# Kernel tuning notes

Measured on AMD Instinct MI355X. Metric: run time of the kernel, lower is better.

Reference implementation:

```python
import jax, jax.numpy as jnp
import numpy as np

IN_FEATURES = 4096
OUT_FEATURES = 4096


def fht(x):
    """Normalized fast Walsh-Hadamard transform along last axis (n = power of 2).
    Equals x @ H_n / sqrt(n); matches matmul_hadU(t)_cuda when had_K is None (K=1)."""
    n = x.shape[-1]
    orig_shape = x.shape
    x = x.reshape(-1, n)
    h = 1
    while h < n:
        x = x.reshape(-1, n // (2 * h), 2, h)
        a = x[:, :, 0, :]
        b = x[:, :, 1, :]
        x = jnp.stack([a + b, a - b], axis=2).reshape(-1, n)
        h *= 2
    scale = jnp.asarray(1.0 / np.sqrt(n), dtype=x.dtype)
    return (x * scale).reshape(orig_shape)


def decode_e8p(Qidxs, grid_abs):
    """E8P12-style decode: each 16-bit codeword -> 8 fp16 weights.
    Low 8 bits index a 256-entry table of 8 absolute values; high 8 bits are
    per-element sign flips. Returns dense W of shape [out, in]."""
    idx = Qidxs.astype(jnp.int32) & 0xFFFF            # [out, in/8]
    abs_vals = grid_abs[idx & 0xFF]                   # [out, in/8, 8]
    sbits = (idx[..., None] >> (8 + jnp.arange(8, dtype=jnp.int32))) & 1
    signs = (1 - 2 * sbits).astype(grid_abs.dtype)    # [out, in/8, 8] in {+1,-1}
    w = abs_vals * signs
    return w.reshape(Qidxs.shape[0], -1)              # [out, in]


def setup_inputs() -> dict:
    key = jax.random.key(0)
    k1, k2, k3, k4, k5, k6 = jax.random.split(key, 6)
    inp = {}
    inp["input"] = jax.random.normal(k1, (2, 4096, IN_FEATURES), dtype=jnp.float16)
    inp["Qidxs"] = jax.random.randint(k2, (OUT_FEATURES, IN_FEATURES // 8), 0, 65536, dtype=jnp.int32)
    # abs half-integer-ish grid values (E8 lattice magnitudes live in ~[0.25, 3.75])
    inp["grid_abs"] = (jax.random.uniform(k3, (256, 8), dtype=jnp.float32) * 3.0 + 0.25).astype(jnp.float16)
    # SU/SV are random sign vectors in QuIP
    inp["SU"] = (1 - 2 * jax.random.bernoulli(k4, 0.5, (IN_FEATURES,)).astype(jnp.float16))
    inp["SV"] = (1 - 2 * jax.random.bernoulli(k5, 0.5, (OUT_FEATURES,)).astype(jnp.float16))
    inp["Wscale"] = jnp.ones((), dtype=jnp.float32)
    inp["bias"] = jax.random.normal(k6, (OUT_FEATURES,), dtype=jnp.float16) * jnp.float16(0.01)
    return inp


def reference(input, Qidxs, grid_abs, SU, SV, Wscale, bias):
    x = input.reshape(-1, input.shape[-1])            # [T, in]
    x = x * SU                                        # input sign rescale
    x = fht(x)                                        # H^T x / sqrt(n) (H symmetric)
    x = (x * Wscale).astype(jnp.float16)              # global weight scale
    W = decode_e8p(Qidxs, grid_abs)                   # [out, in] dequantized lattice weights
    out = jnp.dot(x, W.T, preferred_element_type=jnp.float32).astype(jnp.float16)  # [T, out]
    out = fht(out)                                    # output Hadamard
    out = out * SV + bias                             # output sign rescale + bias
    return out.reshape(*input.shape[:-1], out.shape[-1])
```

## Files before the change

kernel.cpp:

```cpp
#include <hip/hip_runtime.h>
#include <hip/hip_bf16.h>
#include <stdint.h>

typedef _Float16 f16;
typedef _Float16 f16x8 __attribute__((ext_vector_type(8)));
typedef float f32x4 __attribute__((ext_vector_type(4)));

#define N_FEAT 4096
#define M_ROWS 8192
#define QSTRIDE 512

#define GLD16(gptr, lptr)                                                      \
  __builtin_amdgcn_global_load_lds(                                            \
      (const __attribute__((address_space(1))) void*)(gptr),                   \
      (__attribute__((address_space(3))) void*)(uint32_t)(uintptr_t)(lptr),    \
      16, 0, 0)

#define PAD64(i) ((i) + (((i) >> 6) << 2))

__device__ __forceinline__ void fht16(float v[16]) {
#pragma unroll
  for (int h = 1; h < 16; h <<= 1) {
#pragma unroll
    for (int i = 0; i < 16; i += (h << 1)) {
#pragma unroll
      for (int j = 0; j < h; ++j) {
        float a = v[i + j], b = v[i + j + h];
        v[i + j] = a + b;
        v[i + j + h] = a - b;
      }
    }
  }
}

__device__ __forceinline__ void fht16v(f32x4 v[16]) {
#pragma unroll
  for (int h = 1; h < 16; h <<= 1) {
#pragma unroll
    for (int i = 0; i < 16; i += (h << 1)) {
#pragma unroll
      for (int j = 0; j < h; ++j) {
        f32x4 a = v[i + j], b = v[i + j + h];
        v[i + j] = a + b;
        v[i + j + h] = a - b;
      }
    }
  }
}

__device__ __forceinline__ void fht4(float& a, float& b, float& c, float& d) {
  float t0 = a + b, t1 = a - b, t2 = c + d, t3 = c - d;
  a = t0 + t2; b = t1 + t3; c = t0 - t2; d = t1 - t3;
}

#define SWZ(c) ((c) ^ (((((c) >> 4) ^ ((c) >> 8)) & 7) << 2))

__global__ __launch_bounds__(256) void k_fht_in(const float* __restrict__ x,
                                                const float* __restrict__ SU,
                                                const float* __restrict__ wscale,
                                                f16* __restrict__ out) {
  __shared__ __attribute__((aligned(16))) float lds[4 * 4096];
  const int t = threadIdx.x;
  const int rw = t >> 6;
  const int u = t & 63;
  const size_t row = (size_t)blockIdx.x * 4 + rw;
  float* pl = &lds[rw << 12];
  const float* xr = x + row * N_FEAT;

#pragma unroll
  for (int g = 0; g < 4; ++g) {
    const int c16 = (g << 10) + (u << 4);
    float v[16];
#pragma unroll
    for (int q = 0; q < 4; ++q) {
      const f32x4 a = *(const f32x4*)(xr + c16 + (q << 2));
      const f32x4 s4 = *(const f32x4*)(SU + c16 + (q << 2));
      const f32x4 m = a * s4;
      v[4 * q + 0] = m[0]; v[4 * q + 1] = m[1];
      v[4 * q + 2] = m[2]; v[4 * q + 3] = m[3];
    }
    fht16(v);
#pragma unroll
    for (int q = 0; q < 4; ++q) {
      const int col = c16 + (q << 2);
      f32x4 wv = {v[4 * q + 0], v[4 * q + 1], v[4 * q + 2], v[4 * q + 3]};
      *(f32x4*)&pl[SWZ(col)] = wv;
    }
  }
  __syncthreads();

  {
    const int b = u >> 2, a4 = (u & 3) << 2;
    f32x4 v[16];
#pragma unroll
    for (int jj = 0; jj < 16; ++jj)
      v[jj] = *(const f32x4*)&pl[SWZ((b << 8) + (jj << 4) + a4)];
    fht16v(v);
#pragma unroll
    for (int jj = 0; jj < 16; ++jj)
      *(f32x4*)&pl[SWZ((b << 8) + (jj << 4) + a4)] = v[jj];
  }
  __syncthreads();

  {
    const int q4 = u << 2;
    f32x4 v[16];
#pragma unroll
    for (int j = 0; j < 16; ++j)
      v[j] = *(const f32x4*)&pl[SWZ((j << 8) + q4)];
    fht16v(v);
    const float s = wscale[0] * 0.015625f;
    f16* op = out + row * N_FEAT;
#pragma unroll
    for (int j = 0; j < 16; ++j) {
      union { f16 h[4]; uint2 u2; } pk;
      pk.h[0] = (f16)(v[j][0] * s); pk.h[1] = (f16)(v[j][1] * s);
      pk.h[2] = (f16)(v[j][2] * s); pk.h[3] = (f16)(v[j][3] * s);
      *(uint2*)(op + (j << 8) + q4) = pk.u2;
    }
  }
}

__global__ __launch_bounds__(256) void k_wA(const int* __restrict__ q,
                                            const float* __restrict__ grid,
                                            f16* __restrict__ Wp) {
  __shared__ float tabf[2048];
  __shared__ float tile[64 * 65];
  const int t = threadIdx.x;
  const int kg = blockIdx.x;
  const int ng = blockIdx.y;
  {
    *(float4*)&tabf[t * 8] = *(const float4*)(grid + t * 8);
    *(float4*)&tabf[t * 8 + 4] = *(const float4*)(grid + t * 8 + 4);
  }
  __syncthreads();

#pragma unroll
  for (int e2 = 0; e2 < 2; ++e2) {
    const int e = t + (e2 << 8);
    const int nl = e >> 3, c = e & 7;
    const unsigned code =
        (unsigned)q[(size_t)(ng * 64 + nl) * QSTRIDE + kg * 8 + c] & 0xffffu;
    const float* tb = &tabf[(code & 255u) * 8];
#pragma unroll
    for (int j = 0; j < 8; ++j) {
      const int bi = __float_as_int(tb[j]) ^ (int)(((code >> (8 + j)) & 1u) << 31);
      tile[nl * 65 + (c << 3) + j] = __int_as_float(bi);
    }
  }
  __syncthreads();

  {
    const int k = t & 63, p = t >> 6;
    float v[16];
#pragma unroll
    for (int j = 0; j < 16; ++j) v[j] = tile[(16 * p + j) * 65 + k];
    fht16(v);
#pragma unroll
    for (int j = 0; j < 16; ++j) tile[(16 * p + j) * 65 + k] = v[j];
  }
  __syncthreads();

  {
    const int k = t & 63, base = (t >> 6) << 2;
#pragma unroll
    for (int bb = 0; bb < 4; ++bb) {
      const int low = base + bb;
      float v0 = tile[(low) * 65 + k],      v1 = tile[(low + 16) * 65 + k];
      float v2 = tile[(low + 32) * 65 + k], v3 = tile[(low + 48) * 65 + k];
      fht4(v0, v1, v2, v3);
      tile[(low) * 65 + k] = v0;      tile[(low + 16) * 65 + k] = v1;
      tile[(low + 32) * 65 + k] = v2; tile[(low + 48) * 65 + k] = v3;
    }
  }
  __syncthreads();

  {
    const int nl = t >> 2, koff = (t & 3) << 4;
    union { f16 h[16]; int4 v[2]; } u;
#pragma unroll
    for (int i = 0; i < 16; ++i) u.h[i] = (f16)tile[nl * 65 + koff + i];
    int4* dst = (int4*)(Wp + (size_t)(ng * 64 + nl) * N_FEAT + kg * 64 + koff);
    dst[0] = u.v[0];
    dst[1] = u.v[1];
  }
}

__global__ __launch_bounds__(256) void k_wB(f16* __restrict__ Wp) {
  __shared__ float tile[64 * 65];
  const int t = threadIdx.x;
  const int kg = blockIdx.x;
  const int n0 = blockIdx.y;
  {
    const int n1 = t >> 2, koff = (t & 3) << 4;
    const f16* src = Wp + (size_t)(n0 + 64 * n1) * N_FEAT + kg * 64 + koff;
    union { f16 h[16]; int4 v[2]; } u;
    u.v[0] = ((const int4*)src)[0];
    u.v[1] = ((const int4*)src)[1];
#pragma unroll
    for (int i = 0; i < 16; ++i) tile[n1 * 65 + koff + i] = (float)u.h[i];
  }
  __syncthreads();
  {
    const int k = t & 63, p = t >> 6;
    float v[16];
#pragma unroll
    for (int j = 0; j < 16; ++j) v[j] = tile[(16 * p + j) * 65 + k];
    fht16(v);
#pragma unroll
    for (int j = 0; j < 16; ++j) tile[(16 * p + j) * 65 + k] = v[j];
  }
  __syncthreads();
  {
    const int k = t & 63, base = (t >> 6) << 2;
#pragma unroll
    for (int bb = 0; bb < 4; ++bb) {
      const int low = base + bb;
      float v0 = tile[(low) * 65 + k],      v1 = tile[(low + 16) * 65 + k];
      float v2 = tile[(low + 32) * 65 + k], v3 = tile[(low + 48) * 65 + k];
      fht4(v0, v1, v2, v3);
      tile[(low) * 65 + k] = v0;      tile[(low + 16) * 65 + k] = v1;
      tile[(low + 32) * 65 + k] = v2; tile[(low + 48) * 65 + k] = v3;
    }
  }
  __syncthreads();
  {
    const int n1 = t >> 2, koff = (t & 3) << 4;
    union { f16 h[16]; int4 v[2]; } u;
#pragma unroll
    for (int i = 0; i < 16; ++i) u.h[i] = (f16)tile[n1 * 65 + koff + i];
    int4* dst = (int4*)(Wp + (size_t)(n0 + 64 * n1) * N_FEAT + kg * 64 + koff);
    dst[0] = u.v[0];
    dst[1] = u.v[1];
  }
}

#define BM 256
#define BN 256
#define BK 64
#define KDIM 4096

#define WAITB(n)                                          \
  asm volatile("s_waitcnt vmcnt(" #n ")" ::: "memory");   \
  __builtin_amdgcn_s_barrier();

#define SCHED_FENCE() __builtin_amdgcn_sched_barrier(0)

#define STAGE_HALF(gbase, lhalf)                                         \
  {                                                                      \
    _Pragma("unroll")                                                    \
    for (int i_ = 0; i_ < 2; ++i_) {                                     \
      const int rb_ = (w << 4) + (i_ << 3);                              \
      const int r_ = rb_ + srow;                                         \
      const int kc_ = scc ^ (r_ & 7);                                    \
      GLD16((gbase) + (size_t)r_ * KDIM + (kc_ << 3), (lhalf) + (rb_ << 6)); \
    }                                                                    \
  }

#define LDA(dst, mh)                                                     \
  {                                                                      \
    _Pragma("unroll")                                                    \
    for (int i_ = 0; i_ < 4; ++i_) {                                     \
      const int m_ = ((mh) << 7) + (wr << 6) + (i_ << 4) + ml;           \
      _Pragma("unroll")                                                  \
      for (int s_ = 0; s_ < 2; ++s_) {                                   \
        const int kc_ = ((s_ << 2) + quad) ^ (m_ & 7);                   \
        dst[i_][s_] = *(const f16x8*)&sA[cur][(m_ << 6) + (kc_ << 3)];   \
      }                                                                  \
    }                                                                    \
  }

#define LDB(dst, nh)                                                     \
  {                                                                      \
    _Pragma("unroll")                                                    \
    for (int j_ = 0; j_ < 2; ++j_) {                                     \
      const int n_ = ((nh) << 7) + (wc << 5) + (j_ << 4) + ml;           \
      _Pragma("unroll")                                                  \
      for (int s_ = 0; s_ < 2; ++s_) {                                   \
        const int kc_ = ((s_ << 2) + quad) ^ (n_ & 7);                   \
        dst[j_][s_] = *(const f16x8*)&sB[cur][(n_ << 6) + (kc_ << 3)];   \
      }                                                                  \
    }                                                                    \
  }

#define MMAQ(mh, nh, bfx)                                                \
  {                                                                      \
    __builtin_amdgcn_s_setprio(1);                                       \
    _Pragma("unroll")                                                    \
    for (int i_ = 0; i_ < 4; ++i_) {                                     \
      _Pragma("unroll")                                                  \
      for (int j_ = 0; j_ < 2; ++j_) {                                   \
        acc[(mh) * 4 + i_][(nh) * 2 + j_] =                              \
            __builtin_amdgcn_mfma_f32_16x16x32_f16(                      \
                af[i_][0], bfx[j_][0], acc[(mh) * 4 + i_][(nh) * 2 + j_],\
                0, 0, 0);                                                \
        acc[(mh) * 4 + i_][(nh) * 2 + j_] =                              \
            __builtin_amdgcn_mfma_f32_16x16x32_f16(                      \
                af[i_][1], bfx[j_][1], acc[(mh) * 4 + i_][(nh) * 2 + j_],\
                0, 0, 0);                                                \
      }                                                                  \
    }                                                                    \
    __builtin_amdgcn_s_setprio(0);                                       \
  }

__global__ __launch_bounds__(512, 2) void k_gemm(const f16* __restrict__ A,
                                                 const f16* __restrict__ B,
                                                 float* __restrict__ C,
                                                 const float* __restrict__ SV,
                                                 const float* __restrict__ bias) {
  __shared__ __attribute__((aligned(16))) f16 sA[2][BM * BK];
  __shared__ __attribute__((aligned(16))) f16 sB[2][BN * BK];

  const int tid = threadIdx.x;
  const int lane = tid & 63;
  const int w = tid >> 6;
  const int wr = w >> 2;
  const int wc = w & 3;

  const int lin = blockIdx.y * gridDim.x + blockIdx.x;
  const int swz = ((lin & 7) << 6) | (lin >> 3);
  const int m0 = (swz >> 4) * BM;
  const int n0 = (swz & 15) * BN;

  const int quad = lane >> 4;
  const int ml = lane & 15;
  const int srow = lane >> 3;
  const int scc = lane & 7;

  f32x4 acc[8][4];
#pragma unroll
  for (int i = 0; i < 8; ++i)
#pragma unroll
    for (int j = 0; j < 4; ++j) acc[i][j] = (f32x4)0.0f;

  const f16* Ab = A + (size_t)m0 * KDIM;
  const f16* Bb = B + (size_t)n0 * KDIM;

  STAGE_HALF(Ab, &sA[0][0]);
  SCHED_FENCE();
  STAGE_HALF(Bb, &sB[0][0]);
  SCHED_FENCE();
  STAGE_HALF(Bb + (size_t)128 * KDIM, &sB[0][128 * 64]);
  SCHED_FENCE();
  STAGE_HALF(Ab + (size_t)128 * KDIM, &sA[0][128 * 64]);
  WAITB(4);

  f16x8 af[4][2], bflo[2][2], bfhi[2][2];

#pragma unroll 2
  for (int t = 0; t < 64; ++t) {
    const int cur = t & 1;
    const int nxt = cur ^ 1;
    const int kn = ((t + 1) & 63) << 6;
    const f16* An = Ab + kn;
    const f16* Bn = Bb + kn;

    STAGE_HALF(An, &sA[nxt][0]);
    LDA(af, 0);
    LDB(bflo, 0);
    MMAQ(0, 0, bflo);

    WAITB(4);
    STAGE_HALF(Bn, &sB[nxt][0]);
    LDB(bfhi, 1);
    MMAQ(0, 1, bfhi);

    WAITB(4);
    STAGE_HALF(Bn + (size_t)128 * KDIM, &sB[nxt][128 * 64]);
    LDA(af, 1);
    MMAQ(1, 1, bfhi);

    SCHED_FENCE();
    STAGE_HALF(An + (size_t)128 * KDIM, &sA[nxt][128 * 64]);
    MMAQ(1, 0, bflo);
    WAITB(4);
  }

  asm volatile("s_waitcnt vmcnt(0)" ::: "memory");

#pragma unroll
  for (int nj = 0; nj < 4; ++nj) {
    const int col = n0 + ((nj >> 1) << 7) + (wc << 5) + ((nj & 1) << 4) + ml;
    const float sv = SV[col] * 0.015625f;
    const float bs = bias[col];
#pragma unroll
    for (int mi = 0; mi < 8; ++mi) {
      const int rowb =
          m0 + ((mi >> 2) << 7) + (wr << 6) + ((mi & 3) << 4) + (quad << 2);
#pragma unroll
      for (int r = 0; r < 4; ++r)
        C[(size_t)(rowb + r) * N_FEAT + col] = acc[mi][nj][r] * sv + bs;
    }
  }
}

extern "C" void kernel_launch(void* const* d_in, const int* in_sizes, int n_in,
                              void* d_out, int out_size, void* d_ws, size_t ws_size,
                              hipStream_t stream) {
  const float* input = nullptr;
  const int* qidxs = nullptr;
  const float* grid_abs = nullptr;
  const float* wscale = nullptr;
  const float* v4k[3] = {nullptr, nullptr, nullptr};
  int n4 = 0;
  for (int i = 0; i < n_in; ++i) {
    switch (in_sizes[i]) {
      case 33554432: input = (const float*)d_in[i]; break;
      case 2097152:  qidxs = (const int*)d_in[i]; break;
      case 2048:     grid_abs = (const float*)d_in[i]; break;
      case 1:        wscale = (const float*)d_in[i]; break;
      case 4096:     if (n4 < 3) v4k[n4++] = (const float*)d_in[i]; break;
      default: break;
    }
  }
  const float* SU = v4k[0];
  const float* SV = v4k[1];
  const float* bias = v4k[2];

  f16* x = (f16*)d_ws;
  f16* Wp;
  if (ws_size >= (size_t)100663296) {
    Wp = (f16*)((char*)d_ws + 67108864);
  } else {
    Wp = (f16*)const_cast<float*>(input);
  }
  float* out = (float*)d_out;

  k_fht_in<<<M_ROWS / 4, 256, 0, stream>>>(input, SU, wscale, x);
  dim3 gw(64, 64);
  k_wA<<<gw, 256, 0, stream>>>(qidxs, grid_abs, Wp);
  k_wB<<<gw, 256, 0, stream>>>(Wp);
  dim3 g(N_FEAT / BN, M_ROWS / BM);
  k_gemm<<<g, 512, 0, stream>>>(x, Wp, out, SV, bias);
}
```

Measured before the change: 486.6 us.

## Load B fragments directly from global into registers, drop B LDS staging

The GEMM main loop no longer stages the B (weight) tile through shared memory. Each wave loads its B MFMA fragments straight from global memory into double-buffered registers one K-step ahead, and the pipeline is restructured around A-only LDS staging with new vmcnt/barrier points. This halves LDS footprint and traffic and cuts barrier work. In exchange, the 4 column-waves of a block now reload B redundantly from global/L2, registers per thread grow, and vmcnt accounting becomes harder to get right.

Result: slower. 646.2 us (+32.8%).

```diff
diff --git a/kernel.cpp b/kernel.cpp
--- a/kernel.cpp
+++ b/kernel.cpp
@@ -15,8 +15,6 @@
       (const __attribute__((address_space(1))) void*)(gptr),                   \
       (__attribute__((address_space(3))) void*)(uint32_t)(uintptr_t)(lptr),    \
       16, 0, 0)
-
-#define PAD64(i) ((i) + (((i) >> 6) << 2))
 
 __device__ __forceinline__ void fht16(float v[16]) {
 #pragma unroll
@@ -240,10 +238,6 @@
 #define BK 64
 #define KDIM 4096
 
-#define WAITB(n)                                          \
-  asm volatile("s_waitcnt vmcnt(" #n ")" ::: "memory");   \
-  __builtin_amdgcn_s_barrier();
-
 #define SCHED_FENCE() __builtin_amdgcn_sched_barrier(0)
 
 #define STAGE_HALF(gbase, lhalf)                                         \
@@ -257,7 +251,7 @@
     }                                                                    \
   }
 
-#define LDA(dst, mh)                                                     \
+#define LDA(dst, mh, cur)                                                \
   {                                                                      \
     _Pragma("unroll")                                                    \
     for (int i_ = 0; i_ < 4; ++i_) {                                     \
@@ -270,37 +264,56 @@
     }                                                                    \
   }
 
-#define LDB(dst, nh)                                                     \
+#define LOADB(dst, kbase)                                                \
   {                                                                      \
     _Pragma("unroll")                                                    \
-    for (int j_ = 0; j_ < 2; ++j_) {                                     \
-      const int n_ = ((nh) << 7) + (wc << 5) + (j_ << 4) + ml;           \
-      _Pragma("unroll")                                                  \
-      for (int s_ = 0; s_ < 2; ++s_) {                                   \
-        const int kc_ = ((s_ << 2) + quad) ^ (n_ & 7);                   \
-        dst[j_][s_] = *(const f16x8*)&sB[cur][(n_ << 6) + (kc_ << 3)];   \
-      }                                                                  \
+    for (int nj_ = 0; nj_ < 4; ++nj_) {                                  \
+      const int n_ = ((nj_ >> 1) << 7) + (wc << 5) + ((nj_ & 1) << 4) + ml; \
+      const f16* bp_ = Bb + (size_t)n_ * KDIM + (kbase) + (quad << 3);   \
+      dst[nj_][0] = *(const f16x8*)(bp_);                                \
+      dst[nj_][1] = *(const f16x8*)(bp_ + 32);                           \
     }                                                                    \
   }
 
-#define MMAQ(mh, nh, bfx)                                                \
+#define MMAQ2(mh, b)                                                     \
   {                                                                      \
     __builtin_amdgcn_s_setprio(1);                                       \
     _Pragma("unroll")                                                    \
     for (int i_ = 0; i_ < 4; ++i_) {                                     \
       _Pragma("unroll")                                                  \
-      for (int j_ = 0; j_ < 2; ++j_) {                                   \
-        acc[(mh) * 4 + i_][(nh) * 2 + j_] =                              \
+      for (int nj_ = 0; nj_ < 4; ++nj_) {                                \
+        acc[(mh) * 4 + i_][nj_] =                                        \
             __builtin_amdgcn_mfma_f32_16x16x32_f16(                      \
-                af[i_][0], bfx[j_][0], acc[(mh) * 4 + i_][(nh) * 2 + j_],\
-                0, 0, 0);                                                \
-        acc[(mh) * 4 + i_][(nh) * 2 + j_] =                              \
+                af[i_][0], b[nj_][0], acc[(mh) * 4 + i_][nj_], 0, 0, 0); \
+        acc[(mh) * 4 + i_][nj_] =                                        \
             __builtin_amdgcn_mfma_f32_16x16x32_f16(                      \
-                af[i_][1], bfx[j_][1], acc[(mh) * 4 + i_][(nh) * 2 + j_],\
-                0, 0, 0);                                                \
+                af[i_][1], b[nj_][1], acc[(mh) * 4 + i_][nj_], 0, 0, 0); \
       }                                                                  \
     }                                                                    \
     __builtin_amdgcn_s_setprio(0);                                       \
+  }
+
+#define GBODY(bcur, bnxt, tt)                                            \
+  {                                                                      \
+    const int cur_ = (tt) & 1;                                           \
+    const int nxt_ = cur_ ^ 1;                                           \
+    const int kn_ = (((tt) + 1) & 63) << 6;       \
+    const f16* An_ = Ab + kn_;                                           \
+    STAGE_HALF(An_, &sA[nxt_][0]);                               \
+    SCHED_FENCE();                                                       \
+    LDA(af, 0, cur_);                                                    \
+    asm volatile("s_waitcnt vmcnt(4)" ::: "memory");        \
+    MMAQ2(0, bcur);                                                      \
+    LOADB(bnxt, kn_);                                            \
+    SCHED_FENCE();                                                       \
+    asm volatile("s_waitcnt vmcnt(10)" ::: "memory");        \
+    __builtin_amdgcn_s_barrier();                                        \
+    LDA(af, 1, cur_);                                                    \
+    MMAQ2(1, bcur);                                                      \
+    STAGE_HALF(An_ + (size_t)128 * KDIM, &sA[nxt_][128 * 64]);   \
+    SCHED_FENCE();                                                       \
+    asm volatile("s_waitcnt vmcnt(10)" ::: "memory");       \
+    __builtin_amdgcn_s_barrier();                                        \
   }
 
 __global__ __launch_bounds__(512, 2) void k_gemm(const f16* __restrict__ A,
@@ -309,7 +322,6 @@
                                                  const float* __restrict__ SV,
                                                  const float* __restrict__ bias) {
   __shared__ __attribute__((aligned(16))) f16 sA[2][BM * BK];
-  __shared__ __attribute__((aligned(16))) f16 sB[2][BN * BK];
 
   const int tid = threadIdx.x;
   const int lane = tid & 63;
@@ -336,44 +348,20 @@
   const f16* Ab = A + (size_t)m0 * KDIM;
   const f16* Bb = B + (size_t)n0 * KDIM;
 
+  f16x8 af[4][2], bA[4][2], bB[4][2];
+
   STAGE_HALF(Ab, &sA[0][0]);
   SCHED_FENCE();
-  STAGE_HALF(Bb, &sB[0][0]);
-  SCHED_FENCE();
-  STAGE_HALF(Bb + (size_t)128 * KDIM, &sB[0][128 * 64]);
+  LOADB(bA, 0);
   SCHED_FENCE();
   STAGE_HALF(Ab + (size_t)128 * KDIM, &sA[0][128 * 64]);
-  WAITB(4);
-
-  f16x8 af[4][2], bflo[2][2], bfhi[2][2];
-
-#pragma unroll 2
-  for (int t = 0; t < 64; ++t) {
-    const int cur = t & 1;
-    const int nxt = cur ^ 1;
-    const int kn = ((t + 1) & 63) << 6;
-    const f16* An = Ab + kn;
-    const f16* Bn = Bb + kn;
-
-    STAGE_HALF(An, &sA[nxt][0]);
-    LDA(af, 0);
-    LDB(bflo, 0);
-    MMAQ(0, 0, bflo);
-
-    WAITB(4);
-    STAGE_HALF(Bn, &sB[nxt][0]);
-    LDB(bfhi, 1);
-    MMAQ(0, 1, bfhi);
-
-    WAITB(4);
-    STAGE_HALF(Bn + (size_t)128 * KDIM, &sB[nxt][128 * 64]);
-    LDA(af, 1);
-    MMAQ(1, 1, bfhi);
-
-    SCHED_FENCE();
-    STAGE_HALF(An + (size_t)128 * KDIM, &sA[nxt][128 * 64]);
-    MMAQ(1, 0, bflo);
-    WAITB(4);
+  SCHED_FENCE();
+  asm volatile("s_waitcnt vmcnt(10)" ::: "memory");
+  __builtin_amdgcn_s_barrier();
+
+  for (int t2 = 0; t2 < 32; ++t2) {
+    GBODY(bA, bB, 2 * t2);
+    GBODY(bB, bA, 2 * t2 + 1);
   }
 
   asm volatile("s_waitcnt vmcnt(0)" ::: "memory");
```
